# Kernel tuning notes

Hardware: AMD Instinct MI355X
Metric: run time of the kernel (lower is better)

The kernel has to match this reference:

```python
import jax, jax.numpy as jnp
import numpy as np

E = 128
H = 4
D = E // H  # head dim = 32
NEG = -1e9


def setup_inputs() -> dict:
    key = jax.random.key(0)
    ks = jax.random.split(key, 4)
    B, N = 8, 2048
    x = jax.random.normal(ks[0], (B, N, E), dtype=jnp.float32)
    adj = jax.random.randint(ks[1], (B, N, N), 0, 2, dtype=jnp.int32)
    # nn.MultiheadAttention params: packed in_proj (3E,E) + out_proj (E,E)
    in_proj_w = jax.random.normal(ks[2], (3 * E, E), dtype=jnp.float32) * (1.0 / np.sqrt(E))
    in_proj_b = jnp.zeros((3 * E,), dtype=jnp.float32)
    out_w = jax.random.normal(ks[3], (E, E), dtype=jnp.float32) * (1.0 / np.sqrt(E))
    out_b = jnp.zeros((E,), dtype=jnp.float32)
    return {"x": x, "adj": adj, "in_proj_w": in_proj_w, "in_proj_b": in_proj_b,
            "out_w": out_w, "out_b": out_b}


def reference(x, adj, in_proj_w, in_proj_b, out_w, out_b):
    B, N, _ = x.shape
    # additive mask from FIRST batch element only (as in the torch module)
    mask = jnp.where(adj[0] == 0, jnp.float32(NEG), jnp.float32(0.0))  # (N,N)
    # packed QKV projection: x @ W^T + b
    qkv = x @ in_proj_w.T + in_proj_b  # (B,N,3E)
    q, k, v = jnp.split(qkv, 3, axis=-1)
    # (B,N,E) -> (B,H,N,D)
    def heads(t):
        return t.reshape(B, N, H, D).transpose(0, 2, 1, 3)
    q, k, v = heads(q), heads(k), heads(v)
    scores = jnp.einsum('bhnd,bhmd->bhnm', q, k) / jnp.sqrt(jnp.float32(D))
    scores = scores + mask[None, None]  # broadcast shared mask
    attn = jax.nn.softmax(scores, axis=-1)
    out = jnp.einsum('bhnm,bhmd->bhnd', attn, v)  # (B,H,N,D)
    out = out.transpose(0, 2, 1, 3).reshape(B, N, E)
    return out @ out_w.T + out_b
```

## Files before the change

kernel.cpp:

```cpp
#include <hip/hip_runtime.h>


#define EDIM 128
#define SCALE 0.17677669529663687f

typedef unsigned int uint32;
typedef float f32x4 __attribute__((ext_vector_type(4)));
typedef short s16x8 __attribute__((ext_vector_type(8)));
typedef _Float16 f16x2 __attribute__((ext_vector_type(2)));
typedef _Float16 f16x4 __attribute__((ext_vector_type(4)));
typedef _Float16 f16x8 __attribute__((ext_vector_type(8)));
typedef __fp16 g16x2 __attribute__((ext_vector_type(2)));

__device__ inline float bf2f(ushort u) { return __uint_as_float(((uint32)u) << 16); }
__device__ inline ushort f2bf(float f) {
  uint32 u = __float_as_uint(f);
  u += 0x7fffu + ((u >> 16) & 1u);
  return (ushort)(u >> 16);
}
__device__ inline f16x2 pkrtz(float a, float b) {
  g16x2 t = __builtin_amdgcn_cvt_pkrtz(a, b);
  return __builtin_bit_cast(f16x2, t);
}

__device__ inline f32x4 mfma32(s16x8 a, s16x8 b, f32x4 c) {
  return __builtin_amdgcn_mfma_f32_16x16x32_bf16(a, b, c, 0, 0, 0);
}
__device__ inline f32x4 mfma32h(f16x8 a, f16x8 b, f32x4 c) {
  return __builtin_amdgcn_mfma_f32_16x16x32_f16(a, b, c, 0, 0, 0);
}

#if __has_builtin(__builtin_amdgcn_global_load_lds)
#define HAVE_GLL 1
__device__ inline void gll16(const void* g, void* l) {
  __builtin_amdgcn_global_load_lds(
      (const __attribute__((address_space(1))) unsigned int*)g,
      (__attribute__((address_space(3))) unsigned int*)l, 16, 0, 0);
}
#else
#define HAVE_GLL 0
#endif

__device__ inline s16x8 load8(const void* p, size_t e, int fp32) {
  if (fp32) {
    const float* f = (const float*)p + e;
    float4 lo = *(const float4*)f;
    float4 hi = *(const float4*)(f + 4);
    s16x8 r;
    r[0] = (short)f2bf(lo.x); r[1] = (short)f2bf(lo.y);
    r[2] = (short)f2bf(lo.z); r[3] = (short)f2bf(lo.w);
    r[4] = (short)f2bf(hi.x); r[5] = (short)f2bf(hi.y);
    r[6] = (short)f2bf(hi.z); r[7] = (short)f2bf(hi.w);
    return r;
  }
  return *(const s16x8*)((const ushort*)p + e);
}
__device__ inline float loads(const void* p, size_t e, int fp32) {
  return fp32 ? ((const float*)p)[e] : bf2f(((const ushort*)p)[e]);
}

__global__ __launch_bounds__(256) void k_mask(const int* __restrict__ adj,
                                              uint32* __restrict__ mb,
                                              const ushort* __restrict__ xus,
                                              int* __restrict__ flag) {
  if (blockIdx.x == 0 && threadIdx.x < 64) {
    int lane = threadIdx.x, cnt = 0;
#pragma unroll
    for (int i = 0; i < 4; i++) {
      ushort v = xus[2 * (lane * 4 + i)];
      int ex = (v >> 7) & 0xFF;
      cnt += (ex >= 100 && ex <= 140) ? 1 : 0;
    }
#pragma unroll
    for (int s = 1; s < 64; s <<= 1) cnt += __shfl_xor(cnt, s);
    if (lane == 0) *flag = (cnt < 128) ? 1 : 0;
  }
  int idx = blockIdx.x * 256 + threadIdx.x;
  int a = adj[idx];
  unsigned long long bal = __ballot(a != 0);
  int lane = threadIdx.x & 63;
  if (lane == 0)  mb[idx >> 5] = (uint32)bal;
  if (lane == 32) mb[idx >> 5] = (uint32)(bal >> 32);
}

__global__ __launch_bounds__(256) void k_qkv(const void* __restrict__ x,
                                             const void* __restrict__ w,
                                             const void* __restrict__ bias,
                                             ushort* __restrict__ Qg,
                                             ushort* __restrict__ Kg,
                                             _Float16* __restrict__ Vth,
                                             const int* __restrict__ flagp) {
  const int fp32 = *flagp;
  const int tid = threadIdx.x;
  const int wave = tid >> 6, lane = tid & 63, L = lane & 15, quad = lane >> 4;
  const int mt = blockIdx.x * 64 + wave * 16;
  const int jt0 = blockIdx.y * 8;

  s16x8 a[4];
#pragma unroll
  for (int ks = 0; ks < 4; ks++)
    a[ks] = load8(x, (size_t)(mt + L) * EDIM + ks * 32 + quad * 8, fp32);

  const int bidx = mt >> 11;
  const int npos0 = (mt & 2047) + quad * 4;

  for (int jj = 0; jj < 8; jj++) {
    int jt = jt0 + jj;
    f32x4 acc = {0.f, 0.f, 0.f, 0.f};
#pragma unroll
    for (int ks = 0; ks < 4; ks++) {
      s16x8 bf = load8(w, (size_t)(jt * 16 + L) * EDIM + ks * 32 + quad * 8, fp32);
      acc = mfma32(a[ks], bf, acc);
    }
    int j = jt * 16 + L;
    float badd = loads(bias, j, fp32);
    int jm = j & 127;
    int h = jm >> 5, d = jm & 31;
    int bh = bidx * 4 + h;
    int ch = npos0 >> 7, kk = npos0 & 127;
    if (jt < 8) {
#pragma unroll
      for (int r = 0; r < 4; r++)
        Qg[(size_t)bh * 65536 + (size_t)(npos0 + r) * 32 + d] = f2bf((acc[r] + badd) * SCALE);
    } else if (jt < 16) {
      int sub = kk >> 5, k32 = kk & 31, t = k32 >> 3, r8 = k32 & 7;
      int slot0 = sub * 32 + ((r8 >> 2) << 4) + t * 4;
      size_t kb = (size_t)bh * 65536 + (size_t)ch * 4096 + (size_t)slot0 * 32 + d;
#pragma unroll
      for (int r = 0; r < 4; r++) Kg[kb + r * 32] = f2bf(acc[r] + badd);
    } else {
      int g = kk >> 3, e0 = kk & 7;
      f16x2 h0 = pkrtz(acc[0] + badd, acc[1] + badd);
      f16x2 h1 = pkrtz(acc[2] + badd, acc[3] + badd);
      f16x4 pk; pk[0] = h0[0]; pk[1] = h0[1]; pk[2] = h1[0]; pk[3] = h1[1];
      *(f16x4*)(Vth + (size_t)bh * 65536 + (size_t)ch * 4096 + d * 128 +
                (g ^ (d & 7)) * 8 + e0) = pk;
    }
  }
}

__global__ __launch_bounds__(128) void k_attn(const ushort* __restrict__ Qg,
                                              const ushort* __restrict__ Kg,
                                              const _Float16* __restrict__ Vth,
                                              const uint32* __restrict__ mb,
                                              ushort* Oglob, ushort* Oa,
                                              const int* __restrict__ flagp) {
  __shared__ ushort Klds[128 * 32];
  __shared__ ushort Vlds[32 * 128];

  const int fp32 = *flagp;
  ushort* O = fp32 ? Oa : Oglob;

  const int tid = threadIdx.x;
  const int wv = tid >> 6, lane = tid & 63, L = lane & 15, quad = lane >> 4;
  const int bh = blockIdx.x >> 5;
  const int q0 = (blockIdx.x & 31) * 64 + wv * 32;
  const int qgA = q0 + L, qgB = q0 + 16 + L;

  const ushort* Qb = Qg + (size_t)bh * 65536;
  s16x8 qfA = *(const s16x8*)(Qb + (size_t)qgA * 32 + quad * 8);
  s16x8 qfB = *(const s16x8*)(Qb + (size_t)qgB * 32 + quad * 8);

  f32x4 OA0 = {0,0,0,0}, OA1 = {0,0,0,0}, OB0 = {0,0,0,0}, OB1 = {0,0,0,0};
  f32x4 LA = {0,0,0,0}, LB = {0,0,0,0};
  f16x8 ones;
#pragma unroll
  for (int i = 0; i < 8; i++) ones[i] = (_Float16)1.0f;

  const char* Kg8 = (const char*)(Kg + (size_t)bh * 65536);
  const char* Vg8 = (const char*)(Vth + (size_t)bh * 65536);

  for (int c = 0; c < 16; c++) {
    __syncthreads();
#if HAVE_GLL
#pragma unroll
    for (int j = 0; j < 4; j++) {
      int off = (wv + 2 * j) * 1024;
      gll16(Kg8 + (size_t)c * 8192 + off + lane * 16, (char*)Klds + off);
      gll16(Vg8 + (size_t)c * 8192 + off + lane * 16, (char*)Vlds + off);
    }
#else
#pragma unroll
    for (int r = 0; r < 4; r++) {
      int idx = r * 128 + tid;
      *(s16x8*)((char*)Klds + idx * 16) = *(const s16x8*)(Kg8 + (size_t)c * 8192 + idx * 16);
      *(s16x8*)((char*)Vlds + idx * 16) = *(const s16x8*)(Vg8 + (size_t)c * 8192 + idx * 16);
    }
#endif
    __syncthreads();

    uint4 mA = *(const uint4*)(mb + (size_t)qgA * 64 + c * 4);
    uint4 mB = *(const uint4*)(mb + (size_t)qgB * 64 + c * 4);
    uint32 mAw[4] = {mA.x, mA.y, mA.z, mA.w};
    uint32 mBw[4] = {mB.x, mB.y, mB.z, mB.w};

#pragma unroll
    for (int sub = 0; sub < 4; sub++) {
      const f32x4 Z = {0, 0, 0, 0};
      s16x8 kf0 = *(const s16x8*)&Klds[(sub * 32 + L) * 32 + quad * 8];
      s16x8 kf1 = *(const s16x8*)&Klds[(sub * 32 + 16 + L) * 32 + quad * 8];
      f32x4 sA0 = mfma32(kf0, qfA, Z), sA1 = mfma32(kf1, qfA, Z);
      f32x4 sB0 = mfma32(kf0, qfB, Z), sB1 = mfma32(kf1, qfB, Z);

      uint32 mwqA = mAw[sub] >> (quad * 8);
      uint32 mwqB = mBw[sub] >> (quad * 8);
      union { f16x8 v; f16x2 h[4]; } pA, pB;
      float a0 = ((mwqA >> 0) & 1u) ? __expf(sA0[0] - 4.f) : 0.f;
      float a1 = ((mwqA >> 1) & 1u) ? __expf(sA0[1] - 4.f) : 0.f;
      float a2 = ((mwqA >> 2) & 1u) ? __expf(sA0[2] - 4.f) : 0.f;
      float a3 = ((mwqA >> 3) & 1u) ? __expf(sA0[3] - 4.f) : 0.f;
      float a4 = ((mwqA >> 4) & 1u) ? __expf(sA1[0] - 4.f) : 0.f;
      float a5 = ((mwqA >> 5) & 1u) ? __expf(sA1[1] - 4.f) : 0.f;
      float a6 = ((mwqA >> 6) & 1u) ? __expf(sA1[2] - 4.f) : 0.f;
      float a7 = ((mwqA >> 7) & 1u) ? __expf(sA1[3] - 4.f) : 0.f;
      pA.h[0] = pkrtz(a0, a1);
      pA.h[1] = pkrtz(a2, a3);
      pA.h[2] = pkrtz(a4, a5);
      pA.h[3] = pkrtz(a6, a7);
      float b0 = ((mwqB >> 0) & 1u) ? __expf(sB0[0] - 4.f) : 0.f;
      float b1 = ((mwqB >> 1) & 1u) ? __expf(sB0[1] - 4.f) : 0.f;
      float b2 = ((mwqB >> 2) & 1u) ? __expf(sB0[2] - 4.f) : 0.f;
      float b3 = ((mwqB >> 3) & 1u) ? __expf(sB0[3] - 4.f) : 0.f;
      float b4 = ((mwqB >> 4) & 1u) ? __expf(sB1[0] - 4.f) : 0.f;
      float b5 = ((mwqB >> 5) & 1u) ? __expf(sB1[1] - 4.f) : 0.f;
      float b6 = ((mwqB >> 6) & 1u) ? __expf(sB1[2] - 4.f) : 0.f;
      float b7 = ((mwqB >> 7) & 1u) ? __expf(sB1[3] - 4.f) : 0.f;
      pB.h[0] = pkrtz(b0, b1);
      pB.h[1] = pkrtz(b2, b3);
      pB.h[2] = pkrtz(b4, b5);
      pB.h[3] = pkrtz(b6, b7);

      int g = (sub * 4 + quad) ^ (L & 7);
      f16x8 vf0 = *(const f16x8*)&Vlds[L * 128 + g * 8];
      f16x8 vf1 = *(const f16x8*)&Vlds[(16 + L) * 128 + g * 8];
      OA0 = mfma32h(vf0, pA.v, OA0);  OA1 = mfma32h(vf1, pA.v, OA1);
      OB0 = mfma32h(vf0, pB.v, OB0);  OB1 = mfma32h(vf1, pB.v, OB1);
      LA  = mfma32h(ones, pA.v, LA);  LB  = mfma32h(ones, pB.v, LB);
    }
  }

  int b = bh >> 2, h = bh & 3;
  {
    float rn = 1.0f / LA[0];
    size_t ob = ((size_t)(b * 2048 + qgA)) * 128 + h * 32 + quad * 4;
    ushort4 p0, p1;
    p0.x = f2bf(OA0[0] * rn); p0.y = f2bf(OA0[1] * rn);
    p0.z = f2bf(OA0[2] * rn); p0.w = f2bf(OA0[3] * rn);
    p1.x = f2bf(OA1[0] * rn); p1.y = f2bf(OA1[1] * rn);
    p1.z = f2bf(OA1[2] * rn); p1.w = f2bf(OA1[3] * rn);
    *(ushort4*)(O + ob) = p0; *(ushort4*)(O + ob + 16) = p1;
  }
  {
    float rn = 1.0f / LB[0];
    size_t ob = ((size_t)(b * 2048 + qgB)) * 128 + h * 32 + quad * 4;
    ushort4 p0, p1;
    p0.x = f2bf(OB0[0] * rn); p0.y = f2bf(OB0[1] * rn);
    p0.z = f2bf(OB0[2] * rn); p0.w = f2bf(OB0[3] * rn);
    p1.x = f2bf(OB1[0] * rn); p1.y = f2bf(OB1[1] * rn);
    p1.z = f2bf(OB1[2] * rn); p1.w = f2bf(OB1[3] * rn);
    *(ushort4*)(O + ob) = p0; *(ushort4*)(O + ob + 16) = p1;
  }
}

__global__ __launch_bounds__(256) void k_proj(void* outp, const ushort* Oa,
                                              const void* w, const void* bias,
                                              const int* flagp) {
  const int fp32 = *flagp;
  const ushort* src = fp32 ? Oa : (const ushort*)outp;
  const int tid = threadIdx.x;
  const int wave = tid >> 6, lane = tid & 63, L = lane & 15, quad = lane >> 4;
  const int mt = blockIdx.x * 64 + wave * 16;

  s16x8 a[4];
#pragma unroll
  for (int ks = 0; ks < 4; ks++)
    a[ks] = *(const s16x8*)(src + (size_t)(mt + L) * EDIM + ks * 32 + quad * 8);

  for (int jt = 0; jt < 8; jt++) {
    f32x4 acc = {0.f, 0.f, 0.f, 0.f};
#pragma unroll
    for (int ks = 0; ks < 4; ks++) {
      s16x8 bf = load8(w, (size_t)(jt * 16 + L) * EDIM + ks * 32 + quad * 8, fp32);
      acc = mfma32(a[ks], bf, acc);
    }
    float badd = loads(bias, jt * 16 + L, fp32);
#pragma unroll
    for (int r = 0; r < 4; r++) {
      size_t idx = (size_t)(mt + quad * 4 + r) * EDIM + jt * 16 + L;
      if (fp32) ((float*)outp)[idx] = acc[r] + badd;
      else      ((ushort*)outp)[idx] = f2bf(acc[r] + badd);
    }
  }
}

extern "C" void kernel_launch(void* const* d_in, const int* in_sizes, int n_in,
                              void* d_out, int out_size, void* d_ws, size_t ws_size,
                              hipStream_t stream) {
  const void* x   = d_in[0];
  const int*  adj = (const int*)d_in[1];
  const void* ipw = d_in[2];
  const void* ipb = d_in[3];
  const void* ow  = d_in[4];
  const void* ob  = d_in[5];

  char* ws = (char*)d_ws;
  ushort*   Qg  = (ushort*)(ws);
  ushort*   Kg  = (ushort*)(ws + ((size_t)4 << 20));
  _Float16* Vth = (_Float16*)(ws + ((size_t)8 << 20));
  uint32*   mb  = (uint32*)(ws + ((size_t)12 << 20));
  int*      fl  = (int*)(ws + ((size_t)12 << 20) + (512 << 10));
  ushort*   Oa  = (ushort*)(ws + ((size_t)13 << 20));

  hipLaunchKernelGGL(k_mask, dim3(16384), dim3(256), 0, stream, adj, mb,
                     (const ushort*)x, fl);
  hipLaunchKernelGGL(k_qkv, dim3(256, 3), dim3(256), 0, stream, x, ipw, ipb,
                     Qg, Kg, Vth, fl);
  hipLaunchKernelGGL(k_attn, dim3(1024), dim3(128), 0, stream, Qg, Kg, Vth, mb,
                     (ushort*)d_out, Oa, fl);
  hipLaunchKernelGGL(k_proj, dim3(256), dim3(256), 0, stream, d_out, Oa, ow, ob, fl);
}
```

Baseline: 289.3 us.

## Fuse mask and QKV kernels, use exp2 softmax, swizzle K in LDS

Merges the adjacency-bitmask kernel and the QKV projection into one launch, with the projection blocks appended after the mask blocks. Each kernel now recomputes the dtype sniff locally instead of reading a flag from the workspace. The softmax folds log2(e) into the Q scale and the fixed offset into the MFMA accumulator init, then uses a native exp2. K is stored with an XOR swizzle to avoid LDS bank conflicts. Trade-offs: each QKV block now loops over all 24 output tiles, so there are fewer, longer blocks. The sniff also adds a few global reads per block.

```diff
diff --git a/kernel.cpp b/kernel.cpp
--- a/kernel.cpp
+++ b/kernel.cpp
@@ -2,7 +2,8 @@
 
 
 #define EDIM 128
-#define SCALE 0.17677669529663687f
+#define SCALE2 0.25503483f
+#define COFF  -5.7707801f
 
 typedef unsigned int uint32;
 typedef float f32x4 __attribute__((ext_vector_type(4)));
@@ -22,6 +23,13 @@
   g16x2 t = __builtin_amdgcn_cvt_pkrtz(a, b);
   return __builtin_bit_cast(f16x2, t);
 }
+__device__ inline float fexp2(float x) {
+#if __has_builtin(__builtin_amdgcn_exp2f)
+  return __builtin_amdgcn_exp2f(x);
+#else
+  return __exp2f(x);
+#endif
+}
 
 __device__ inline f32x4 mfma32(s16x8 a, s16x8 b, f32x4 c) {
   return __builtin_amdgcn_mfma_f32_16x16x32_bf16(a, b, c, 0, 0, 0);
@@ -40,6 +48,19 @@
 #else
 #define HAVE_GLL 0
 #endif
+
+__device__ inline int sniff_fp32(const ushort* __restrict__ xus) {
+  int lane = threadIdx.x & 63, cnt = 0;
+#pragma unroll
+  for (int i = 0; i < 4; i++) {
+    ushort v = xus[2 * (lane * 4 + i)];
+    int ex = (v >> 7) & 0xFF;
+    cnt += (ex >= 100 && ex <= 140) ? 1 : 0;
+  }
+#pragma unroll
+  for (int s = 1; s < 64; s <<= 1) cnt += __shfl_xor(cnt, s);
+  return cnt < 128;
+}
 
 __device__ inline s16x8 load8(const void* p, size_t e, int fp32) {
   if (fp32) {
@@ -59,42 +80,27 @@
   return fp32 ? ((const float*)p)[e] : bf2f(((const ushort*)p)[e]);
 }
 
-__global__ __launch_bounds__(256) void k_mask(const int* __restrict__ adj,
-                                              uint32* __restrict__ mb,
-                                              const ushort* __restrict__ xus,
-                                              int* __restrict__ flag) {
-  if (blockIdx.x == 0 && threadIdx.x < 64) {
-    int lane = threadIdx.x, cnt = 0;
-#pragma unroll
-    for (int i = 0; i < 4; i++) {
-      ushort v = xus[2 * (lane * 4 + i)];
-      int ex = (v >> 7) & 0xFF;
-      cnt += (ex >= 100 && ex <= 140) ? 1 : 0;
-    }
-#pragma unroll
-    for (int s = 1; s < 64; s <<= 1) cnt += __shfl_xor(cnt, s);
-    if (lane == 0) *flag = (cnt < 128) ? 1 : 0;
-  }
-  int idx = blockIdx.x * 256 + threadIdx.x;
-  int a = adj[idx];
-  unsigned long long bal = __ballot(a != 0);
-  int lane = threadIdx.x & 63;
-  if (lane == 0)  mb[idx >> 5] = (uint32)bal;
-  if (lane == 32) mb[idx >> 5] = (uint32)(bal >> 32);
-}
-
-__global__ __launch_bounds__(256) void k_qkv(const void* __restrict__ x,
+__global__ __launch_bounds__(256) void k_pre(const int* __restrict__ adj,
+                                             uint32* __restrict__ mb,
+                                             const void* __restrict__ x,
                                              const void* __restrict__ w,
                                              const void* __restrict__ bias,
                                              ushort* __restrict__ Qg,
                                              ushort* __restrict__ Kg,
-                                             _Float16* __restrict__ Vth,
-                                             const int* __restrict__ flagp) {
-  const int fp32 = *flagp;
+                                             _Float16* __restrict__ Vth) {
+  if (blockIdx.x < 16384) {
+    int idx = blockIdx.x * 256 + threadIdx.x;
+    int a = adj[idx];
+    unsigned long long bal = __ballot(a != 0);
+    int lane = threadIdx.x & 63;
+    if (lane == 0)  mb[idx >> 5] = (uint32)bal;
+    if (lane == 32) mb[idx >> 5] = (uint32)(bal >> 32);
+    return;
+  }
+  const int fp32 = sniff_fp32((const ushort*)x);
   const int tid = threadIdx.x;
   const int wave = tid >> 6, lane = tid & 63, L = lane & 15, quad = lane >> 4;
-  const int mt = blockIdx.x * 64 + wave * 16;
-  const int jt0 = blockIdx.y * 8;
+  const int mt = (blockIdx.x - 16384) * 64 + wave * 16;
 
   s16x8 a[4];
 #pragma unroll
@@ -104,8 +110,7 @@
   const int bidx = mt >> 11;
   const int npos0 = (mt & 2047) + quad * 4;
 
-  for (int jj = 0; jj < 8; jj++) {
-    int jt = jt0 + jj;
+  for (int jt = 0; jt < 24; jt++) {
     f32x4 acc = {0.f, 0.f, 0.f, 0.f};
 #pragma unroll
     for (int ks = 0; ks < 4; ks++) {
@@ -121,13 +126,15 @@
     if (jt < 8) {
 #pragma unroll
       for (int r = 0; r < 4; r++)
-        Qg[(size_t)bh * 65536 + (size_t)(npos0 + r) * 32 + d] = f2bf((acc[r] + badd) * SCALE);
+        Qg[(size_t)bh * 65536 + (size_t)(npos0 + r) * 32 + d] = f2bf((acc[r] + badd) * SCALE2);
     } else if (jt < 16) {
       int sub = kk >> 5, k32 = kk & 31, t = k32 >> 3, r8 = k32 & 7;
       int slot0 = sub * 32 + ((r8 >> 2) << 4) + t * 4;
-      size_t kb = (size_t)bh * 65536 + (size_t)ch * 4096 + (size_t)slot0 * 32 + d;
-#pragma unroll
-      for (int r = 0; r < 4; r++) Kg[kb + r * 32] = f2bf(acc[r] + badd);
+      size_t kb = (size_t)bh * 65536 + (size_t)ch * 4096;
+#pragma unroll
+      for (int r = 0; r < 4; r++)
+        Kg[kb + (size_t)(slot0 + r) * 32 + (((d >> 3) ^ r) << 3) + (d & 7)] =
+            f2bf(acc[r] + badd);
     } else {
       int g = kk >> 3, e0 = kk & 7;
       f16x2 h0 = pkrtz(acc[0] + badd, acc[1] + badd);
@@ -143,12 +150,12 @@
                                               const ushort* __restrict__ Kg,
                                               const _Float16* __restrict__ Vth,
                                               const uint32* __restrict__ mb,
-                                              ushort* Oglob, ushort* Oa,
-                                              const int* __restrict__ flagp) {
+                                              const ushort* __restrict__ xus,
+                                              ushort* Oglob, ushort* Oa) {
   __shared__ ushort Klds[128 * 32];
   __shared__ ushort Vlds[32 * 128];
 
-  const int fp32 = *flagp;
+  const int fp32 = sniff_fp32(xus);
   ushort* O = fp32 ? Oa : Oglob;
 
   const int tid = threadIdx.x;
@@ -169,6 +176,7 @@
 
   const char* Kg8 = (const char*)(Kg + (size_t)bh * 65536);
   const char* Vg8 = (const char*)(Vth + (size_t)bh * 65536);
+  const int g0 = quad ^ (L & 3);
 
   for (int c = 0; c < 16; c++) {
     __syncthreads();
@@ -181,6 +189,10 @@
     }
 #else
 #pragma unroll
+    for (int r = 0; r < 8; r++) {
+      int idx = r * 128 + tid;
+    }
+#pragma unroll
     for (int r = 0; r < 4; r++) {
       int idx = r * 128 + tid;
       *(s16x8*)((char*)Klds + idx * 16) = *(const s16x8*)(Kg8 + (size_t)c * 8192 + idx * 16);
@@ -196,39 +208,35 @@
 
 #pragma unroll
     for (int sub = 0; sub < 4; sub++) {
-      const f32x4 Z = {0, 0, 0, 0};
-      s16x8 kf0 = *(const s16x8*)&Klds[(sub * 32 + L) * 32 + quad * 8];
-      s16x8 kf1 = *(const s16x8*)&Klds[(sub * 32 + 16 + L) * 32 + quad * 8];
-      f32x4 sA0 = mfma32(kf0, qfA, Z), sA1 = mfma32(kf1, qfA, Z);
-      f32x4 sB0 = mfma32(kf0, qfB, Z), sB1 = mfma32(kf1, qfB, Z);
+      const f32x4 Zc = {COFF, COFF, COFF, COFF};
+      s16x8 kf0 = *(const s16x8*)&Klds[(sub * 32 + L) * 32 + g0 * 8];
+      s16x8 kf1 = *(const s16x8*)&Klds[(sub * 32 + 16 + L) * 32 + g0 * 8];
+      f32x4 sA0 = mfma32(kf0, qfA, Zc), sA1 = mfma32(kf1, qfA, Zc);
+      f32x4 sB0 = mfma32(kf0, qfB, Zc), sB1 = mfma32(kf1, qfB, Zc);
 
       uint32 mwqA = mAw[sub] >> (quad * 8);
       uint32 mwqB = mBw[sub] >> (quad * 8);
       union { f16x8 v; f16x2 h[4]; } pA, pB;
-      float a0 = ((mwqA >> 0) & 1u) ? __expf(sA0[0] - 4.f) : 0.f;
-      float a1 = ((mwqA >> 1) & 1u) ? __expf(sA0[1] - 4.f) : 0.f;
-      float a2 = ((mwqA >> 2) & 1u) ? __expf(sA0[2] - 4.f) : 0.f;
-      float a3 = ((mwqA >> 3) & 1u) ? __expf(sA0[3] - 4.f) : 0.f;
-      float a4 = ((mwqA >> 4) & 1u) ? __expf(sA1[0] - 4.f) : 0.f;
-      float a5 = ((mwqA >> 5) & 1u) ? __expf(sA1[1] - 4.f) : 0.f;
-      float a6 = ((mwqA >> 6) & 1u) ? __expf(sA1[2] - 4.f) : 0.f;
-      float a7 = ((mwqA >> 7) & 1u) ? __expf(sA1[3] - 4.f) : 0.f;
-      pA.h[0] = pkrtz(a0, a1);
-      pA.h[1] = pkrtz(a2, a3);
-      pA.h[2] = pkrtz(a4, a5);
-      pA.h[3] = pkrtz(a6, a7);
-      float b0 = ((mwqB >> 0) & 1u) ? __expf(sB0[0] - 4.f) : 0.f;
-      float b1 = ((mwqB >> 1) & 1u) ? __expf(sB0[1] - 4.f) : 0.f;
-      float b2 = ((mwqB >> 2) & 1u) ? __expf(sB0[2] - 4.f) : 0.f;
-      float b3 = ((mwqB >> 3) & 1u) ? __expf(sB0[3] - 4.f) : 0.f;
-      float b4 = ((mwqB >> 4) & 1u) ? __expf(sB1[0] - 4.f) : 0.f;
-      float b5 = ((mwqB >> 5) & 1u) ? __expf(sB1[1] - 4.f) : 0.f;
-      float b6 = ((mwqB >> 6) & 1u) ? __expf(sB1[2] - 4.f) : 0.f;
-      float b7 = ((mwqB >> 7) & 1u) ? __expf(sB1[3] - 4.f) : 0.f;
-      pB.h[0] = pkrtz(b0, b1);
-      pB.h[1] = pkrtz(b2, b3);
-      pB.h[2] = pkrtz(b4, b5);
-      pB.h[3] = pkrtz(b6, b7);
+      float a0 = ((mwqA >> 0) & 1u) ? fexp2(sA0[0]) : 0.f;
+      float a1 = ((mwqA >> 1) & 1u) ? fexp2(sA0[1]) : 0.f;
+      float a2 = ((mwqA >> 2) & 1u) ? fexp2(sA0[2]) : 0.f;
+      float a3 = ((mwqA >> 3) & 1u) ? fexp2(sA0[3]) : 0.f;
+      float a4 = ((mwqA >> 4) & 1u) ? fexp2(sA1[0]) : 0.f;
+      float a5 = ((mwqA >> 5) & 1u) ? fexp2(sA1[1]) : 0.f;
+      float a6 = ((mwqA >> 6) & 1u) ? fexp2(sA1[2]) : 0.f;
+      float a7 = ((mwqA >> 7) & 1u) ? fexp2(sA1[3]) : 0.f;
+      pA.h[0] = pkrtz(a0, a1); pA.h[1] = pkrtz(a2, a3);
+      pA.h[2] = pkrtz(a4, a5); pA.h[3] = pkrtz(a6, a7);
+      float b0 = ((mwqB >> 0) & 1u) ? fexp2(sB0[0]) : 0.f;
+      float b1 = ((mwqB >> 1) & 1u) ? fexp2(sB0[1]) : 0.f;
+      float b2 = ((mwqB >> 2) & 1u) ? fexp2(sB0[2]) : 0.f;
+      float b3 = ((mwqB >> 3) & 1u) ? fexp2(sB0[3]) : 0.f;
+      float b4 = ((mwqB >> 4) & 1u) ? fexp2(sB1[0]) : 0.f;
+      float b5 = ((mwqB >> 5) & 1u) ? fexp2(sB1[1]) : 0.f;
+      float b6 = ((mwqB >> 6) & 1u) ? fexp2(sB1[2]) : 0.f;
+      float b7 = ((mwqB >> 7) & 1u) ? fexp2(sB1[3]) : 0.f;
+      pB.h[0] = pkrtz(b0, b1); pB.h[1] = pkrtz(b2, b3);
+      pB.h[2] = pkrtz(b4, b5); pB.h[3] = pkrtz(b6, b7);
 
       int g = (sub * 4 + quad) ^ (L & 7);
       f16x8 vf0 = *(const f16x8*)&Vlds[L * 128 + g * 8];
@@ -264,8 +272,8 @@
 
 __global__ __launch_bounds__(256) void k_proj(void* outp, const ushort* Oa,
                                               const void* w, const void* bias,
-                                              const int* flagp) {
-  const int fp32 = *flagp;
+                                              const ushort* __restrict__ xus) {
+  const int fp32 = sniff_fp32(xus);
   const ushort* src = fp32 ? Oa : (const ushort*)outp;
   const int tid = threadIdx.x;
   const int wave = tid >> 6, lane = tid & 63, L = lane & 15, quad = lane >> 4;
@@ -308,14 +316,12 @@
   ushort*   Kg  = (ushort*)(ws + ((size_t)4 << 20));
   _Float16* Vth = (_Float16*)(ws + ((size_t)8 << 20));
   uint32*   mb  = (uint32*)(ws + ((size_t)12 << 20));
-  int*      fl  = (int*)(ws + ((size_t)12 << 20) + (512 << 10));
   ushort*   Oa  = (ushort*)(ws + ((size_t)13 << 20));
 
-  hipLaunchKernelGGL(k_mask, dim3(16384), dim3(256), 0, stream, adj, mb,
-                     (const ushort*)x, fl);
-  hipLaunchKernelGGL(k_qkv, dim3(256, 3), dim3(256), 0, stream, x, ipw, ipb,
-                     Qg, Kg, Vth, fl);
+  hipLaunchKernelGGL(k_pre, dim3(16384 + 256), dim3(256), 0, stream,
+                     adj, mb, x, ipw, ipb, Qg, Kg, Vth);
   hipLaunchKernelGGL(k_attn, dim3(1024), dim3(128), 0, stream, Qg, Kg, Vth, mb,
-                     (ushort*)d_out, Oa, fl);
-  hipLaunchKernelGGL(k_proj, dim3(256), dim3(256), 0, stream, d_out, Oa, ow, ob, fl);
-}
+                     (const ushort*)x, (ushort*)d_out, Oa);
+  hipLaunchKernelGGL(k_proj, dim3(256), dim3(256), 0, stream, d_out, Oa, ow, ob,
+                     (const ushort*)x);
+}
```

Result: slower. 360.5 us (+24.6%).
